# Kernel optimization log

Measured on AMD Instinct MI355X. Metric: run time of the kernel, lower is better.

Reference implementation:

```python
import jax, jax.numpy as jnp
import numpy as np

INPUT_NDIMS = 1024
HIDDEN = 512
LATENT = 50
BATCH = 16384

def setup_inputs() -> dict:
    key = jax.random.key(0)
    ks = jax.random.split(key, 12)
    s = 0.02
    x = jax.random.uniform(ks[0], (BATCH, INPUT_NDIMS), dtype=jnp.float32)
    u = 0.01 + 0.98 * jax.random.uniform(ks[1], (BATCH, LATENT), dtype=jnp.float32)
    W1 = s * jax.random.normal(ks[2], (HIDDEN, INPUT_NDIMS), dtype=jnp.float32)
    b1 = jnp.zeros((HIDDEN,), jnp.float32)
    Wa = s * jax.random.normal(ks[3], (LATENT, HIDDEN), dtype=jnp.float32)
    ba = jnp.zeros((LATENT,), jnp.float32)
    Wb = s * jax.random.normal(ks[4], (LATENT, HIDDEN), dtype=jnp.float32)
    bb = jnp.zeros((LATENT,), jnp.float32)
    W2 = s * jax.random.normal(ks[5], (HIDDEN, LATENT), dtype=jnp.float32)
    b2 = jnp.zeros((HIDDEN,), jnp.float32)
    W3 = s * jax.random.normal(ks[6], (INPUT_NDIMS, HIDDEN), dtype=jnp.float32)
    b3 = jnp.zeros((INPUT_NDIMS,), jnp.float32)
    return dict(x=x, u=u, W1=W1, b1=b1, Wa=Wa, ba=ba, Wb=Wb, bb=bb, W2=W2, b2=b2, W3=W3, b3=b3)

def _stick_segments(v):
    # pi[:, k] = v[:, k] * prod_{j<k} (1 - v[:, j])  -- single O(K) cumprod pass
    cp = jnp.cumprod(1.0 - v, axis=1)                       # inclusive cumprod
    excl = jnp.concatenate([jnp.ones_like(cp[:, :1]), cp[:, :-1]], axis=1)
    return v * excl

def reference(x, u, W1, b1, Wa, ba, Wb, bb, W2, b2, W3, b3):
    # encoder: MLP -> positive Kumaraswamy params alpha (param1), beta (param2)
    h = jax.nn.relu(x @ W1.T + b1)                           # [B, H]
    alpha = jax.nn.softplus(h @ Wa.T + ba) + 1e-4            # [B, K]
    beta = jax.nn.softplus(h @ Wb.T + bb) + 1e-4             # [B, K]
    # Kumaraswamy reparameterized sample: v = (1 - u^(1/beta))^(1/alpha)
    v = jnp.power(1.0 - jnp.power(u, 1.0 / beta), 1.0 / alpha)
    # set_v_K_to_one: force last stick fraction to 1 so segments sum to 1
    v = v.at[:, -1].set(1.0)
    pi = _stick_segments(v)                                  # [B, K], rows sum to 1
    # decoder: MLP with sigmoid output
    h2 = jax.nn.relu(pi @ W2.T + b2)                         # [B, H]
    recon = jax.nn.sigmoid(h2 @ W3.T + b3)                   # [B, D]
    return recon, alpha, beta
```

## Files before the change

### kernel.cpp

```cpp
#include <hip/hip_runtime.h>
#include <hip/hip_bf16.h>

typedef __hip_bfloat16 bf16_t;
typedef __attribute__((ext_vector_type(4))) float f32x4;
typedef __attribute__((ext_vector_type(8))) __bf16 bf16x8;
typedef __attribute__((ext_vector_type(8))) short s16x8;
typedef __attribute__((ext_vector_type(4))) unsigned short u16x4;

#define BATCH 16384
#define NDIM  1024
#define HID   512
#define LAT   50

#define LOG2E 1.44269504088896340736f
#define RLOG2E 0.69314718055994530942f

__device__ __forceinline__ float ex2(float x) { return __builtin_amdgcn_exp2f(x); }
__device__ __forceinline__ float lg2(float x) { return __builtin_amdgcn_logf(x); }
__device__ __forceinline__ float rcp(float x) { return __builtin_amdgcn_rcpf(x); }

__device__ inline unsigned short f2b_u(float f) {
  union { bf16_t b; unsigned short u; } cv; cv.b = __float2bfloat16(f); return cv.u;
}

__device__ __forceinline__ void gload16(const void* src, void* dst_lds) {
  __builtin_amdgcn_global_load_lds(
      reinterpret_cast<const __attribute__((address_space(1))) void*>(
          reinterpret_cast<unsigned long long>(src)),
      reinterpret_cast<__attribute__((address_space(3))) void*>(
          static_cast<unsigned>(reinterpret_cast<unsigned long long>(dst_lds))),
      16, 0, 0);
}

#define WAIT_VMCNT(N)                                          \
  do {                                                         \
    asm volatile("s_waitcnt vmcnt(%0)" ::"i"(N) : "memory");   \
    __builtin_amdgcn_sched_barrier(0);                         \
  } while (0)
#define WAIT_LGKM0                                             \
  do {                                                         \
    asm volatile("s_waitcnt lgkmcnt(0)" ::: "memory");         \
    __builtin_amdgcn_sched_barrier(0);                         \
  } while (0)

__global__ void prep_w_kernel(const float* __restrict__ W1, const float* __restrict__ W3,
                              const float* __restrict__ Wa, const float* __restrict__ Wb,
                              const float* __restrict__ W2, const float* __restrict__ ba,
                              const float* __restrict__ bb,
                              bf16_t* __restrict__ w1, bf16_t* __restrict__ w3,
                              bf16_t* __restrict__ wab, bf16_t* __restrict__ w2p,
                              float* __restrict__ bab)
{
  const int W1U  = (HID * NDIM) / 4;
  const int W3U  = (NDIM * HID) / 4;
  const int WABN = 128 * HID;
  const int W2PN = HID * 64;
  const int TOT  = W1U + W3U + WABN + W2PN + 128;
  for (int i = blockIdx.x * blockDim.x + threadIdx.x; i < TOT;
       i += gridDim.x * blockDim.x) {
    int j = i;
    if (j < W1U) {
      const f32x4 v = ((const f32x4*)W1)[j];
      u16x4 o; o[0]=f2b_u(v[0]); o[1]=f2b_u(v[1]); o[2]=f2b_u(v[2]); o[3]=f2b_u(v[3]);
      ((u16x4*)w1)[j] = o; continue;
    }
    j -= W1U;
    if (j < W3U) {
      const f32x4 v = ((const f32x4*)W3)[j];
      u16x4 o; o[0]=f2b_u(v[0]); o[1]=f2b_u(v[1]); o[2]=f2b_u(v[2]); o[3]=f2b_u(v[3]);
      ((u16x4*)w3)[j] = o; continue;
    }
    j -= W3U;
    if (j < WABN) {
      const int n = j >> 9, k = j & 511;
      float v = (n < 50) ? Wa[n * 512 + k] : ((n < 100) ? Wb[(n - 50) * 512 + k] : 0.f);
      wab[j] = __float2bfloat16(v); continue;
    }
    j -= WABN;
    if (j < W2PN) {
      const int n = j >> 6, k = j & 63;
      w2p[j] = __float2bfloat16(k < 50 ? W2[n * 50 + k] : 0.f); continue;
    }
    j -= W2PN;
    bab[j] = (j < 50) ? ba[j] : ((j < 100) ? bb[j - 50] : 0.f);
  }
}

template<int A_F32, int EPI, int BM>
__global__ __launch_bounds__(512, 1)
void gemm256_kernel(const void* __restrict__ Av, const bf16_t* __restrict__ B,
                    const float* __restrict__ bias, void* __restrict__ out0,
                    int M, int N, int K)
{
  constexpr int BN  = 256;
  constexpr int BUF = (BM + BN) * 128;
  constexpr int RA  = BM / 64;
  constexpr int MI  = BM / 32;
  constexpr int FPQ = MI / 4;
  __shared__ char lds[2 * BUF];

  const int tid  = threadIdx.x;
  const int swzid = ((blockIdx.x & 7) * (gridDim.x >> 3)) + (blockIdx.x >> 3);
  const int nblocks = N / BN;
  const int bn   = swzid % nblocks;
  const int bm   = swzid / nblocks;
  const int wid  = tid >> 6;
  const int lane = tid & 63;
  const int l15  = lane & 15;
  const int l4   = lane >> 4;
  const int wm   = (wid >> 2) * (BM / 2);
  const int wn   = (wid & 3) * 64;
  const int uw   = __builtin_amdgcn_readfirstlane(wid);

  f32x4 acc[MI][4] = {};
  f32x4 areg[4];

  auto stage_A_round = [&](char* buf, int k0, int i) {
    const bf16_t* A = (const bf16_t*)Av;
    const int c  = (i * 8 + uw) * 64 + lane;
    const int r  = c >> 3;
    const int sp = c & 7;
    const int sl = sp ^ (r & 7);
    gload16(A + (size_t)(bm * BM + r) * K + k0 + sl * 8,
            buf + (i * 8 + uw) * 1024);
  };
  auto stage_B_round = [&](char* buf, int k0, int i) {
    char* lB = buf + BM * 128;
    const int c  = (i * 8 + uw) * 64 + lane;
    const int r  = c >> 3;
    const int sp = c & 7;
    const int sl = sp ^ (r & 7);
    gload16(B + (size_t)(bn * BN + r) * K + k0 + sl * 8,
            lB + (i * 8 + uw) * 1024);
  };
  auto load_A_f32 = [&](int k0) {
    const float* A = (const float*)Av;
    #pragma unroll
    for (int j = 0; j < 2; ++j) {
      const int c  = j * 512 + tid;
      const int r  = c >> 3;
      const int sl = c & 7;
      const float* s = A + (size_t)(bm * BM + r) * K + k0 + sl * 8;
      areg[2 * j]     = *(const f32x4*)s;
      areg[2 * j + 1] = *(const f32x4*)(s + 4);
    }
  };
  auto write_A_f32 = [&](char* buf) {
    #pragma unroll
    for (int j = 0; j < 2; ++j) {
      const int c  = j * 512 + tid;
      const int r  = c >> 3;
      const int sl = c & 7;
      const int sp = sl ^ (r & 7);
      union { s16x8 v; unsigned short us[8]; } o;
      const f32x4 v0 = areg[2 * j], v1 = areg[2 * j + 1];
      o.us[0]=f2b_u(v0[0]); o.us[1]=f2b_u(v0[1]); o.us[2]=f2b_u(v0[2]); o.us[3]=f2b_u(v0[3]);
      o.us[4]=f2b_u(v1[0]); o.us[5]=f2b_u(v1[1]); o.us[6]=f2b_u(v1[2]); o.us[7]=f2b_u(v1[3]);
      *(s16x8*)(buf + r * 128 + sp * 16) = o.v;
    }
  };

  const int nt = K >> 6;
  if constexpr (A_F32) {
    load_A_f32(0); write_A_f32(lds);
  } else {
    #pragma unroll
    for (int i = 0; i < RA; ++i) stage_A_round(lds, 0, i);
  }
  #pragma unroll
  for (int i = 0; i < 4; ++i) stage_B_round(lds, 0, i);
  WAIT_VMCNT(0);
  if (A_F32) WAIT_LGKM0;
  __builtin_amdgcn_s_barrier();

  for (int t = 0; t < nt; ++t) {
    char* buf  = lds + (t & 1) * BUF;
    char* nbuf = lds + ((t + 1) & 1) * BUF;
    const char* lA = buf;
    const char* lB = buf + BM * 128;
    const bool pf  = (t + 1 < nt);
    const int k0n  = (t + 1) << 6;

    if (pf) {
      if constexpr (A_F32) {
        load_A_f32(k0n);
      } else {
        #pragma unroll
        for (int i = 0; i < RA; ++i) stage_A_round(nbuf, k0n, i);
      }
      #pragma unroll
      for (int i = 0; i < 4; ++i) stage_B_round(nbuf, k0n, i);
    }

    bf16x8 bfr[4][2];
    #pragma unroll
    for (int ni = 0; ni < 4; ++ni)
      #pragma unroll
      for (int h = 0; h < 2; ++h) {
        const int row = wn + ni * 16 + l15;
        const int sp  = (h * 4 + l4) ^ (row & 7);
        bfr[ni][h] = *(const bf16x8*)(lB + row * 128 + sp * 16);
      }

    #pragma unroll
    for (int q = 0; q < 4; ++q) {
      bf16x8 af[FPQ][2];
      #pragma unroll
      for (int f = 0; f < FPQ; ++f)
        #pragma unroll
        for (int h = 0; h < 2; ++h) {
          const int row = wm + (q * FPQ + f) * 16 + l15;
          const int sp  = (h * 4 + l4) ^ (row & 7);
          af[f][h] = *(const bf16x8*)(lA + row * 128 + sp * 16);
        }
      __builtin_amdgcn_s_setprio(1);
      #pragma unroll
      for (int f = 0; f < FPQ; ++f)
        #pragma unroll
        for (int ni = 0; ni < 4; ++ni)
          #pragma unroll
          for (int h = 0; h < 2; ++h)
            acc[q * FPQ + f][ni] = __builtin_amdgcn_mfma_f32_16x16x32_bf16(
                af[f][h], bfr[ni][h], acc[q * FPQ + f][ni], 0, 0, 0);
      __builtin_amdgcn_s_setprio(0);
    }

    if (A_F32 && pf) write_A_f32(nbuf);
    WAIT_VMCNT(0);
    if (A_F32) WAIT_LGKM0;
    __builtin_amdgcn_s_barrier();
  }

  #pragma unroll
  for (int ni = 0; ni < 4; ++ni) {
    const int n  = bn * BN + wn + ni * 16 + l15;
    const float bv = bias[n];
    #pragma unroll
    for (int mi = 0; mi < MI; ++mi) {
      #pragma unroll
      for (int r = 0; r < 4; ++r) {
        const int m  = bm * BM + wm + mi * 16 + l4 * 4 + r;
        const float t = acc[mi][ni][r] + bv;
        if (EPI == 0) {
          ((bf16_t*)out0)[(size_t)m * N + n] = __float2bfloat16(fmaxf(t, 0.f));
        } else {
          ((float*)out0)[(size_t)m * N + n] = rcp(1.f + ex2(-t * LOG2E));
        }
      }
    }
  }
}

__global__ __launch_bounds__(512, 1)
void abstick_kernel(const bf16_t* __restrict__ A, const bf16_t* __restrict__ wabg,
                    const float* __restrict__ bab, const bf16_t* __restrict__ w2pg,
                    const float* __restrict__ b2, const float* __restrict__ u,
                    float* __restrict__ out_a, float* __restrict__ out_b,
                    bf16_t* __restrict__ h2)
{
  constexpr int BUF = 64 * 128 + 16384;
  constexpr int PIL = 65536;
  constexpr int SMO = 73728;
  __shared__ char lds[100352];

  const int tid  = threadIdx.x;
  const int swzid = ((blockIdx.x & 7) * (gridDim.x >> 3)) + (blockIdx.x >> 3);
  const int bm   = swzid;
  const int wid  = tid >> 6;
  const int lane = tid & 63;
  const int l15  = lane & 15;
  const int l4   = lane >> 4;
  const int wm   = (wid >> 2) * 32;
  const int wn   = (wid & 3) * 32;
  const int uw   = __builtin_amdgcn_readfirstlane(wid);
  const int K    = HID;

  f32x4 acc[2][2] = {};

  auto stage_AB = [&](char* buf, int k0) {
    {
      const int c  = tid;
      const int r  = c >> 3;
      const int sp = c & 7;
      const int sl = sp ^ (r & 7);
      gload16(A + (size_t)(bm * 64 + r) * K + k0 + sl * 8, buf + uw * 1024);
    }
    char* lB = buf + 8192;
    #pragma unroll
    for (int i = 0; i < 2; ++i) {
      const int c  = (i * 8 + uw) * 64 + lane;
      const int r  = c >> 3;
      const int sp = c & 7;
      const int sl = sp ^ (r & 7);
      gload16(wabg + (size_t)r * K + k0 + sl * 8, lB + (i * 8 + uw) * 1024);
    }
  };
  auto compute1 = [&](const char* buf) {
    const char* lA = buf;
    const char* lB = buf + 8192;
    #pragma unroll
    for (int h = 0; h < 2; ++h) {
      bf16x8 af[2], bfr[2];
      #pragma unroll
      for (int mi = 0; mi < 2; ++mi) {
        const int row = wm + mi * 16 + l15;
        const int sp  = (h * 4 + l4) ^ (row & 7);
        af[mi] = *(const bf16x8*)(lA + row * 128 + sp * 16);
      }
      #pragma unroll
      for (int ni = 0; ni < 2; ++ni) {
        const int row = wn + ni * 16 + l15;
        const int sp  = (h * 4 + l4) ^ (row & 7);
        bfr[ni] = *(const bf16x8*)(lB + row * 128 + sp * 16);
      }
      #pragma unroll
      for (int mi = 0; mi < 2; ++mi)
        #pragma unroll
        for (int ni = 0; ni < 2; ++ni)
          acc[mi][ni] = __builtin_amdgcn_mfma_f32_16x16x32_bf16(
              af[mi], bfr[ni], acc[mi][ni], 0, 0, 0);
    }
  };

  stage_AB(lds, 0);
  stage_AB(lds + BUF, 64);
  for (int t = 0; t < 8; ++t) {
    if (t + 1 < 8) WAIT_VMCNT(3);
    else           WAIT_VMCNT(0);
    __builtin_amdgcn_s_barrier();
    compute1(lds + (t & 1) * BUF);
    __builtin_amdgcn_s_barrier();
    __builtin_amdgcn_sched_barrier(0);
    if (t + 2 < 8) stage_AB(lds + (t & 1) * BUF, (t + 2) << 6);
  }

  const int ul = (lane < 49) ? lane : 0;
  float ureg[8];
  #pragma unroll
  for (int rr = 0; rr < 8; ++rr) {
    const size_t m = (size_t)(bm * 64 + wid * 8 + rr);
    ureg[rr] = u[m * 50 + ul];
  }

  #pragma unroll
  for (int i = 0; i < 8; ++i) {
    const int c  = (i * 8 + uw) * 64 + lane;
    const int r  = c >> 3;
    const int sp = c & 7;
    const int sl = sp ^ (r & 7);
    gload16(w2pg + (size_t)r * 64 + sl * 8, lds + (i * 8 + uw) * 1024);
  }

  float* sm = (float*)(lds + SMO);
  #pragma unroll
  for (int ni = 0; ni < 2; ++ni) {
    const int n  = wn + ni * 16 + l15;
    const float bv = bab[n];
    #pragma unroll
    for (int mi = 0; mi < 2; ++mi) {
      #pragma unroll
      for (int r = 0; r < 4; ++r) {
        const int ml = wm + mi * 16 + l4 * 4 + r;
        const int m  = bm * 64 + ml;
        const float t = acc[mi][ni][r] + bv;
        if (n < 100) {
          const float y =
              (t > 20.f ? t : lg2(1.f + ex2(t * LOG2E)) * RLOG2E) + 1e-4f;
          if (n < 50) out_a[(size_t)m * 50 + n] = y;
          else        out_b[(size_t)m * 50 + (n - 50)] = y;
          sm[ml * 104 + n + (n < 50 ? 0 : 2)] = y;
        }
      }
    }
  }
  __syncthreads();

  #pragma unroll 1
  for (int rr = 0; rr < 8; ++rr) {
    const int rl = wid * 8 + rr;
    const size_t m = (size_t)(bm * 64 + rl);
    float v = 1.f, t = 1.f;
    if (lane < 49) {
      const float a  = sm[rl * 104 + lane];
      const float b  = sm[rl * 104 + 52 + lane];
      const float uu = ureg[rr];
      const float tb = ex2(lg2(uu) * rcp(b));
      v = ex2(lg2(1.f - tb) * rcp(a));
      t = 1.f - v;
    }
    float p = t;
    #pragma unroll
    for (int d = 1; d < 64; d <<= 1) {
      const float o = __shfl_up(p, d, 64);
      if (lane >= d) p *= o;
    }
    float e = __shfl_up(p, 1, 64);
    if (lane == 0) e = 1.f;
    const float piv = (lane < 50) ? v * e : 0.f;
    *(unsigned short*)(lds + PIL + rl * 128 +
                       (((lane >> 3) ^ (rl & 7)) << 4) + ((lane & 7) << 1)) =
        f2b_u(piv);
  }
  __syncthreads();

  const int wn3 = (wid & 3) * 128;
  f32x4 acc3[2][8] = {};
  #pragma unroll
  for (int h = 0; h < 2; ++h) {
    bf16x8 af[2], bfr[8];
    #pragma unroll
    for (int mi = 0; mi < 2; ++mi) {
      const int row = wm + mi * 16 + l15;
      const int sp  = (h * 4 + l4) ^ (row & 7);
      af[mi] = *(const bf16x8*)(lds + PIL + row * 128 + sp * 16);
    }
    #pragma unroll
    for (int ni = 0; ni < 8; ++ni) {
      const int row = wn3 + ni * 16 + l15;
      const int sp  = (h * 4 + l4) ^ (row & 7);
      bfr[ni] = *(const bf16x8*)(lds + row * 128 + sp * 16);
    }
    #pragma unroll
    for (int mi = 0; mi < 2; ++mi)
      #pragma unroll
      for (int ni = 0; ni < 8; ++ni)
        acc3[mi][ni] = __builtin_amdgcn_mfma_f32_16x16x32_bf16(
            af[mi], bfr[ni], acc3[mi][ni], 0, 0, 0);
  }
  #pragma unroll
  for (int ni = 0; ni < 8; ++ni) {
    const int n  = wn3 + ni * 16 + l15;
    const float bv = b2[n];
    #pragma unroll
    for (int mi = 0; mi < 2; ++mi) {
      #pragma unroll
      for (int r = 0; r < 4; ++r) {
        const int m  = bm * 64 + wm + mi * 16 + l4 * 4 + r;
        h2[(size_t)m * HID + n] =
            __float2bfloat16(fmaxf(acc3[mi][ni][r] + bv, 0.f));
      }
    }
  }
}

extern "C" void kernel_launch(void* const* d_in, const int* in_sizes, int n_in,
                              void* d_out, int out_size, void* d_ws, size_t ws_size,
                              hipStream_t stream)
{
  const float* x  = (const float*)d_in[0];
  const float* u  = (const float*)d_in[1];
  const float* W1 = (const float*)d_in[2];
  const float* b1 = (const float*)d_in[3];
  const float* Wa = (const float*)d_in[4];
  const float* ba = (const float*)d_in[5];
  const float* Wb = (const float*)d_in[6];
  const float* bb = (const float*)d_in[7];
  const float* W2 = (const float*)d_in[8];
  const float* b2 = (const float*)d_in[9];
  const float* W3 = (const float*)d_in[10];
  const float* b3 = (const float*)d_in[11];

  float* recon  = (float*)d_out;
  float* oalpha = recon + (size_t)BATCH * NDIM;
  float* obeta  = oalpha + (size_t)BATCH * LAT;

  char* ws = (char*)d_ws;
  bf16_t* h2  = (bf16_t*)(ws);
  bf16_t* h   = (bf16_t*)(ws + 16777216);
  bf16_t* w1  = (bf16_t*)(ws + 33554432);
  bf16_t* w3  = (bf16_t*)(ws + 34603008);
  bf16_t* wab = (bf16_t*)(ws + 35651584);
  bf16_t* w2p = (bf16_t*)(ws + 35782656);
  float*  bab = (float*)(ws + 35848192);

  prep_w_kernel<<<512, 256, 0, stream>>>(W1, W3, Wa, Wb, W2, ba, bb,
                                         w1, w3, wab, w2p, bab);
  gemm256_kernel<1, 0, 128><<<256, 512, 0, stream>>>(
      x, w1, b1, (void*)h, BATCH, HID, NDIM);
  abstick_kernel<<<256, 512, 0, stream>>>(
      h, wab, bab, w2p, b2, u, oalpha, obeta, h2);
  gemm256_kernel<0, 1, 256><<<256, 512, 0, stream>>>(
      h2, w3, b3, (void*)recon, BATCH, NDIM, HID);
}
```

Measured before the change: 78.19 us.

## Merge four kernels into one cooperative persistent kernel with grid syncs

Replaces the weight-prep, first GEMM, alpha/beta+stick-breaking, and output GEMM launches with a single cooperative kernel that separates the phases with grid.sync(). The aim is to remove per-launch overhead and inter-kernel gaps. The cost is grid-wide barriers and a larger fixed LDS allocation (128 KB) shared across all phases. The weight prep phase now runs on 256 blocks of 512 threads instead of 512 blocks of 256.

```diff
diff --git a/kernel.cpp b/kernel.cpp
--- a/kernel.cpp
+++ b/kernel.cpp
@@ -1,5 +1,8 @@
 #include <hip/hip_runtime.h>
 #include <hip/hip_bf16.h>
+#include <hip/hip_cooperative_groups.h>
+
+namespace cg = cooperative_groups;
 
 typedef __hip_bfloat16 bf16_t;
 typedef __attribute__((ext_vector_type(4))) float f32x4;
@@ -43,63 +46,18 @@
     __builtin_amdgcn_sched_barrier(0);                         \
   } while (0)
 
-__global__ void prep_w_kernel(const float* __restrict__ W1, const float* __restrict__ W3,
-                              const float* __restrict__ Wa, const float* __restrict__ Wb,
-                              const float* __restrict__ W2, const float* __restrict__ ba,
-                              const float* __restrict__ bb,
-                              bf16_t* __restrict__ w1, bf16_t* __restrict__ w3,
-                              bf16_t* __restrict__ wab, bf16_t* __restrict__ w2p,
-                              float* __restrict__ bab)
-{
-  const int W1U  = (HID * NDIM) / 4;
-  const int W3U  = (NDIM * HID) / 4;
-  const int WABN = 128 * HID;
-  const int W2PN = HID * 64;
-  const int TOT  = W1U + W3U + WABN + W2PN + 128;
-  for (int i = blockIdx.x * blockDim.x + threadIdx.x; i < TOT;
-       i += gridDim.x * blockDim.x) {
-    int j = i;
-    if (j < W1U) {
-      const f32x4 v = ((const f32x4*)W1)[j];
-      u16x4 o; o[0]=f2b_u(v[0]); o[1]=f2b_u(v[1]); o[2]=f2b_u(v[2]); o[3]=f2b_u(v[3]);
-      ((u16x4*)w1)[j] = o; continue;
-    }
-    j -= W1U;
-    if (j < W3U) {
-      const f32x4 v = ((const f32x4*)W3)[j];
-      u16x4 o; o[0]=f2b_u(v[0]); o[1]=f2b_u(v[1]); o[2]=f2b_u(v[2]); o[3]=f2b_u(v[3]);
-      ((u16x4*)w3)[j] = o; continue;
-    }
-    j -= W3U;
-    if (j < WABN) {
-      const int n = j >> 9, k = j & 511;
-      float v = (n < 50) ? Wa[n * 512 + k] : ((n < 100) ? Wb[(n - 50) * 512 + k] : 0.f);
-      wab[j] = __float2bfloat16(v); continue;
-    }
-    j -= WABN;
-    if (j < W2PN) {
-      const int n = j >> 6, k = j & 63;
-      w2p[j] = __float2bfloat16(k < 50 ? W2[n * 50 + k] : 0.f); continue;
-    }
-    j -= W2PN;
-    bab[j] = (j < 50) ? ba[j] : ((j < 100) ? bb[j - 50] : 0.f);
-  }
-}
-
 template<int A_F32, int EPI, int BM>
-__global__ __launch_bounds__(512, 1)
-void gemm256_kernel(const void* __restrict__ Av, const bf16_t* __restrict__ B,
-                    const float* __restrict__ bias, void* __restrict__ out0,
-                    int M, int N, int K)
+__device__ __forceinline__
+void gemm_phase(const void* __restrict__ Av, const bf16_t* __restrict__ B,
+                const float* __restrict__ bias, void* __restrict__ out0,
+                int N, int K, char* lds, int tid)
 {
   constexpr int BN  = 256;
   constexpr int BUF = (BM + BN) * 128;
   constexpr int RA  = BM / 64;
   constexpr int MI  = BM / 32;
   constexpr int FPQ = MI / 4;
-  __shared__ char lds[2 * BUF];
-
-  const int tid  = threadIdx.x;
+
   const int swzid = ((blockIdx.x & 7) * (gridDim.x >> 3)) + (blockIdx.x >> 3);
   const int nblocks = N / BN;
   const int bn   = swzid % nblocks;
@@ -252,195 +210,247 @@
 }
 
 __global__ __launch_bounds__(512, 1)
-void abstick_kernel(const bf16_t* __restrict__ A, const bf16_t* __restrict__ wabg,
-                    const float* __restrict__ bab, const bf16_t* __restrict__ w2pg,
-                    const float* __restrict__ b2, const float* __restrict__ u,
-                    float* __restrict__ out_a, float* __restrict__ out_b,
-                    bf16_t* __restrict__ h2)
+void mega_kernel(const float* __restrict__ x, const float* __restrict__ u,
+                 const float* __restrict__ W1, const float* __restrict__ b1,
+                 const float* __restrict__ Wa, const float* __restrict__ ba,
+                 const float* __restrict__ Wb, const float* __restrict__ bb,
+                 const float* __restrict__ W2, const float* __restrict__ b2,
+                 const float* __restrict__ W3, const float* __restrict__ b3,
+                 float* __restrict__ recon, float* __restrict__ oalpha,
+                 float* __restrict__ obeta, bf16_t* __restrict__ h,
+                 bf16_t* __restrict__ h2, bf16_t* __restrict__ w1,
+                 bf16_t* __restrict__ w3, bf16_t* __restrict__ wab,
+                 bf16_t* __restrict__ w2p, float* __restrict__ bab)
 {
-  constexpr int BUF = 64 * 128 + 16384;
-  constexpr int PIL = 65536;
-  constexpr int SMO = 73728;
-  __shared__ char lds[100352];
-
-  const int tid  = threadIdx.x;
-  const int swzid = ((blockIdx.x & 7) * (gridDim.x >> 3)) + (blockIdx.x >> 3);
-  const int bm   = swzid;
-  const int wid  = tid >> 6;
-  const int lane = tid & 63;
-  const int l15  = lane & 15;
-  const int l4   = lane >> 4;
-  const int wm   = (wid >> 2) * 32;
-  const int wn   = (wid & 3) * 32;
-  const int uw   = __builtin_amdgcn_readfirstlane(wid);
-  const int K    = HID;
-
-  f32x4 acc[2][2] = {};
-
-  auto stage_AB = [&](char* buf, int k0) {
-    {
-      const int c  = tid;
-      const int r  = c >> 3;
-      const int sp = c & 7;
-      const int sl = sp ^ (r & 7);
-      gload16(A + (size_t)(bm * 64 + r) * K + k0 + sl * 8, buf + uw * 1024);
-    }
-    char* lB = buf + 8192;
-    #pragma unroll
-    for (int i = 0; i < 2; ++i) {
+  cg::grid_group grid = cg::this_grid();
+  __shared__ char lds[131072];
+  const int tid = threadIdx.x;
+
+  {
+    const int W1U  = (HID * NDIM) / 4;
+    const int W3U  = (NDIM * HID) / 4;
+    const int WABN = 128 * HID;
+    const int W2PN = HID * 64;
+    const int TOT  = W1U + W3U + WABN + W2PN + 128;
+    for (int i = blockIdx.x * blockDim.x + tid; i < TOT;
+         i += gridDim.x * blockDim.x) {
+      int j = i;
+      if (j < W1U) {
+        const f32x4 v = ((const f32x4*)W1)[j];
+        u16x4 o; o[0]=f2b_u(v[0]); o[1]=f2b_u(v[1]); o[2]=f2b_u(v[2]); o[3]=f2b_u(v[3]);
+        ((u16x4*)w1)[j] = o; continue;
+      }
+      j -= W1U;
+      if (j < W3U) {
+        const f32x4 v = ((const f32x4*)W3)[j];
+        u16x4 o; o[0]=f2b_u(v[0]); o[1]=f2b_u(v[1]); o[2]=f2b_u(v[2]); o[3]=f2b_u(v[3]);
+        ((u16x4*)w3)[j] = o; continue;
+      }
+      j -= W3U;
+      if (j < WABN) {
+        const int n = j >> 9, k = j & 511;
+        float v = (n < 50) ? Wa[n * 512 + k] : ((n < 100) ? Wb[(n - 50) * 512 + k] : 0.f);
+        wab[j] = __float2bfloat16(v); continue;
+      }
+      j -= WABN;
+      if (j < W2PN) {
+        const int n = j >> 6, k = j & 63;
+        w2p[j] = __float2bfloat16(k < 50 ? W2[n * 50 + k] : 0.f); continue;
+      }
+      j -= W2PN;
+      bab[j] = (j < 50) ? ba[j] : ((j < 100) ? bb[j - 50] : 0.f);
+    }
+  }
+  grid.sync();
+
+  gemm_phase<1, 0, 128>(x, w1, b1, (void*)h, HID, NDIM, lds, tid);
+  grid.sync();
+
+  {
+    constexpr int BUF = 64 * 128 + 16384;
+    constexpr int PIL = 65536;
+    constexpr int SMO = 73728;
+    const bf16_t* A = h;
+    const int swzid = ((blockIdx.x & 7) * (gridDim.x >> 3)) + (blockIdx.x >> 3);
+    const int bm   = swzid;
+    const int wid  = tid >> 6;
+    const int lane = tid & 63;
+    const int l15  = lane & 15;
+    const int l4   = lane >> 4;
+    const int wm   = (wid >> 2) * 32;
+    const int wn   = (wid & 3) * 32;
+    const int uw   = __builtin_amdgcn_readfirstlane(wid);
+    const int K    = HID;
+
+    f32x4 acc[2][2] = {};
+
+    auto stage_AB = [&](char* buf, int k0) {
+      {
+        const int c  = tid;
+        const int r  = c >> 3;
+        const int sp = c & 7;
+        const int sl = sp ^ (r & 7);
+        gload16(A + (size_t)(bm * 64 + r) * K + k0 + sl * 8, buf + uw * 1024);
+      }
+      char* lB = buf + 8192;
+      #pragma unroll
+      for (int i = 0; i < 2; ++i) {
+        const int c  = (i * 8 + uw) * 64 + lane;
+        const int r  = c >> 3;
+        const int sp = c & 7;
+        const int sl = sp ^ (r & 7);
+        gload16(wab + (size_t)r * K + k0 + sl * 8, lB + (i * 8 + uw) * 1024);
+      }
+    };
+    auto compute1 = [&](const char* buf) {
+      const char* lA = buf;
+      const char* lB = buf + 8192;
+      #pragma unroll
+      for (int hh = 0; hh < 2; ++hh) {
+        bf16x8 af[2], bfr[2];
+        #pragma unroll
+        for (int mi = 0; mi < 2; ++mi) {
+          const int row = wm + mi * 16 + l15;
+          const int sp  = (hh * 4 + l4) ^ (row & 7);
+          af[mi] = *(const bf16x8*)(lA + row * 128 + sp * 16);
+        }
+        #pragma unroll
+        for (int ni = 0; ni < 2; ++ni) {
+          const int row = wn + ni * 16 + l15;
+          const int sp  = (hh * 4 + l4) ^ (row & 7);
+          bfr[ni] = *(const bf16x8*)(lB + row * 128 + sp * 16);
+        }
+        #pragma unroll
+        for (int mi = 0; mi < 2; ++mi)
+          #pragma unroll
+          for (int ni = 0; ni < 2; ++ni)
+            acc[mi][ni] = __builtin_amdgcn_mfma_f32_16x16x32_bf16(
+                af[mi], bfr[ni], acc[mi][ni], 0, 0, 0);
+      }
+    };
+
+    stage_AB(lds, 0);
+    stage_AB(lds + BUF, 64);
+    for (int t = 0; t < 8; ++t) {
+      if (t + 1 < 8) WAIT_VMCNT(3);
+      else           WAIT_VMCNT(0);
+      __builtin_amdgcn_s_barrier();
+      compute1(lds + (t & 1) * BUF);
+      __builtin_amdgcn_s_barrier();
+      __builtin_amdgcn_sched_barrier(0);
+      if (t + 2 < 8) stage_AB(lds + (t & 1) * BUF, (t + 2) << 6);
+    }
+
+    const int ul = (lane < 49) ? lane : 0;
+    float ureg[8];
+    #pragma unroll
+    for (int rr = 0; rr < 8; ++rr) {
+      const size_t m = (size_t)(bm * 64 + wid * 8 + rr);
+      ureg[rr] = u[m * 50 + ul];
+    }
+
+    #pragma unroll
+    for (int i = 0; i < 8; ++i) {
       const int c  = (i * 8 + uw) * 64 + lane;
       const int r  = c >> 3;
       const int sp = c & 7;
       const int sl = sp ^ (r & 7);
-      gload16(wabg + (size_t)r * K + k0 + sl * 8, lB + (i * 8 + uw) * 1024);
-    }
-  };
-  auto compute1 = [&](const char* buf) {
-    const char* lA = buf;
-    const char* lB = buf + 8192;
-    #pragma unroll
-    for (int h = 0; h < 2; ++h) {
-      bf16x8 af[2], bfr[2];
+      gload16(w2p + (size_t)r * 64 + sl * 8, lds + (i * 8 + uw) * 1024);
+    }
+
+    float* sm = (float*)(lds + SMO);
+    #pragma unroll
+    for (int ni = 0; ni < 2; ++ni) {
+      const int n  = wn + ni * 16 + l15;
+      const float bv = bab[n];
+      #pragma unroll
+      for (int mi = 0; mi < 2; ++mi) {
+        #pragma unroll
+        for (int r = 0; r < 4; ++r) {
+          const int ml = wm + mi * 16 + l4 * 4 + r;
+          const int m  = bm * 64 + ml;
+          const float t = acc[mi][ni][r] + bv;
+          if (n < 100) {
+            const float y =
+                (t > 20.f ? t : lg2(1.f + ex2(t * LOG2E)) * RLOG2E) + 1e-4f;
+            if (n < 50) oalpha[(size_t)m * 50 + n] = y;
+            else        obeta[(size_t)m * 50 + (n - 50)] = y;
+            sm[ml * 104 + n + (n < 50 ? 0 : 2)] = y;
+          }
+        }
+      }
+    }
+    __syncthreads();
+
+    #pragma unroll 1
+    for (int rr = 0; rr < 8; ++rr) {
+      const int rl = wid * 8 + rr;
+      float v = 1.f, t = 1.f;
+      if (lane < 49) {
+        const float a  = sm[rl * 104 + lane];
+        const float b  = sm[rl * 104 + 52 + lane];
+        const float uu = ureg[rr];
+        const float tb = ex2(lg2(uu) * rcp(b));
+        v = ex2(lg2(1.f - tb) * rcp(a));
+        t = 1.f - v;
+      }
+      float p = t;
+      #pragma unroll
+      for (int d = 1; d < 64; d <<= 1) {
+        const float o = __shfl_up(p, d, 64);
+        if (lane >= d) p *= o;
+      }
+      float e = __shfl_up(p, 1, 64);
+      if (lane == 0) e = 1.f;
+      const float piv = (lane < 50) ? v * e : 0.f;
+      *(unsigned short*)(lds + PIL + rl * 128 +
+                         (((lane >> 3) ^ (rl & 7)) << 4) + ((lane & 7) << 1)) =
+          f2b_u(piv);
+    }
+    __syncthreads();
+
+    const int wn3 = (wid & 3) * 128;
+    f32x4 acc3[2][8] = {};
+    #pragma unroll
+    for (int hh = 0; hh < 2; ++hh) {
+      bf16x8 af[2], bfr[8];
       #pragma unroll
       for (int mi = 0; mi < 2; ++mi) {
         const int row = wm + mi * 16 + l15;
-        const int sp  = (h * 4 + l4) ^ (row & 7);
-        af[mi] = *(const bf16x8*)(lA + row * 128 + sp * 16);
-      }
-      #pragma unroll
-      for (int ni = 0; ni < 2; ++ni) {
-        const int row = wn + ni * 16 + l15;
-        const int sp  = (h * 4 + l4) ^ (row & 7);
-        bfr[ni] = *(const bf16x8*)(lB + row * 128 + sp * 16);
+        const int sp  = (hh * 4 + l4) ^ (row & 7);
+        af[mi] = *(const bf16x8*)(lds + PIL + row * 128 + sp * 16);
+      }
+      #pragma unroll
+      for (int ni = 0; ni < 8; ++ni) {
+        const int row = wn3 + ni * 16 + l15;
+        const int sp  = (hh * 4 + l4) ^ (row & 7);
+        bfr[ni] = *(const bf16x8*)(lds + row * 128 + sp * 16);
       }
       #pragma unroll
       for (int mi = 0; mi < 2; ++mi)
         #pragma unroll
-        for (int ni = 0; ni < 2; ++ni)
-          acc[mi][ni] = __builtin_amdgcn_mfma_f32_16x16x32_bf16(
-              af[mi], bfr[ni], acc[mi][ni], 0, 0, 0);
-    }
-  };
-
-  stage_AB(lds, 0);
-  stage_AB(lds + BUF, 64);
-  for (int t = 0; t < 8; ++t) {
-    if (t + 1 < 8) WAIT_VMCNT(3);
-    else           WAIT_VMCNT(0);
-    __builtin_amdgcn_s_barrier();
-    compute1(lds + (t & 1) * BUF);
-    __builtin_amdgcn_s_barrier();
-    __builtin_amdgcn_sched_barrier(0);
-    if (t + 2 < 8) stage_AB(lds + (t & 1) * BUF, (t + 2) << 6);
+        for (int ni = 0; ni < 8; ++ni)
+          acc3[mi][ni] = __builtin_amdgcn_mfma_f32_16x16x32_bf16(
+              af[mi], bfr[ni], acc3[mi][ni], 0, 0, 0);
+    }
+    #pragma unroll
+    for (int ni = 0; ni < 8; ++ni) {
+      const int n  = wn3 + ni * 16 + l15;
+      const float bv = b2[n];
+      #pragma unroll
+      for (int mi = 0; mi < 2; ++mi) {
+        #pragma unroll
+        for (int r = 0; r < 4; ++r) {
+          const int m  = bm * 64 + wm + mi * 16 + l4 * 4 + r;
+          h2[(size_t)m * HID + n] =
+              __float2bfloat16(fmaxf(acc3[mi][ni][r] + bv, 0.f));
+        }
+      }
+    }
   }
-
-  const int ul = (lane < 49) ? lane : 0;
-  float ureg[8];
-  #pragma unroll
-  for (int rr = 0; rr < 8; ++rr) {
-    const size_t m = (size_t)(bm * 64 + wid * 8 + rr);
-    ureg[rr] = u[m * 50 + ul];
-  }
-
-  #pragma unroll
-  for (int i = 0; i < 8; ++i) {
-    const int c  = (i * 8 + uw) * 64 + lane;
-    const int r  = c >> 3;
-    const int sp = c & 7;
-    const int sl = sp ^ (r & 7);
-    gload16(w2pg + (size_t)r * 64 + sl * 8, lds + (i * 8 + uw) * 1024);
-  }
-
-  float* sm = (float*)(lds + SMO);
-  #pragma unroll
-  for (int ni = 0; ni < 2; ++ni) {
-    const int n  = wn + ni * 16 + l15;
-    const float bv = bab[n];
-    #pragma unroll
-    for (int mi = 0; mi < 2; ++mi) {
-      #pragma unroll
-      for (int r = 0; r < 4; ++r) {
-        const int ml = wm + mi * 16 + l4 * 4 + r;
-        const int m  = bm * 64 + ml;
-        const float t = acc[mi][ni][r] + bv;
-        if (n < 100) {
-          const float y =
-              (t > 20.f ? t : lg2(1.f + ex2(t * LOG2E)) * RLOG2E) + 1e-4f;
-          if (n < 50) out_a[(size_t)m * 50 + n] = y;
-          else        out_b[(size_t)m * 50 + (n - 50)] = y;
-          sm[ml * 104 + n + (n < 50 ? 0 : 2)] = y;
-        }
-      }
-    }
-  }
-  __syncthreads();
-
-  #pragma unroll 1
-  for (int rr = 0; rr < 8; ++rr) {
-    const int rl = wid * 8 + rr;
-    const size_t m = (size_t)(bm * 64 + rl);
-    float v = 1.f, t = 1.f;
-    if (lane < 49) {
-      const float a  = sm[rl * 104 + lane];
-      const float b  = sm[rl * 104 + 52 + lane];
-      const float uu = ureg[rr];
-      const float tb = ex2(lg2(uu) * rcp(b));
-      v = ex2(lg2(1.f - tb) * rcp(a));
-      t = 1.f - v;
-    }
-    float p = t;
-    #pragma unroll
-    for (int d = 1; d < 64; d <<= 1) {
-      const float o = __shfl_up(p, d, 64);
-      if (lane >= d) p *= o;
-    }
-    float e = __shfl_up(p, 1, 64);
-    if (lane == 0) e = 1.f;
-    const float piv = (lane < 50) ? v * e : 0.f;
-    *(unsigned short*)(lds + PIL + rl * 128 +
-                       (((lane >> 3) ^ (rl & 7)) << 4) + ((lane & 7) << 1)) =
-        f2b_u(piv);
-  }
-  __syncthreads();
-
-  const int wn3 = (wid & 3) * 128;
-  f32x4 acc3[2][8] = {};
-  #pragma unroll
-  for (int h = 0; h < 2; ++h) {
-    bf16x8 af[2], bfr[8];
-    #pragma unroll
-    for (int mi = 0; mi < 2; ++mi) {
-      const int row = wm + mi * 16 + l15;
-      const int sp  = (h * 4 + l4) ^ (row & 7);
-      af[mi] = *(const bf16x8*)(lds + PIL + row * 128 + sp * 16);
-    }
-    #pragma unroll
-    for (int ni = 0; ni < 8; ++ni) {
-      const int row = wn3 + ni * 16 + l15;
-      const int sp  = (h * 4 + l4) ^ (row & 7);
-      bfr[ni] = *(const bf16x8*)(lds + row * 128 + sp * 16);
-    }
-    #pragma unroll
-    for (int mi = 0; mi < 2; ++mi)
-      #pragma unroll
-      for (int ni = 0; ni < 8; ++ni)
-        acc3[mi][ni] = __builtin_amdgcn_mfma_f32_16x16x32_bf16(
-            af[mi], bfr[ni], acc3[mi][ni], 0, 0, 0);
-  }
-  #pragma unroll
-  for (int ni = 0; ni < 8; ++ni) {
-    const int n  = wn3 + ni * 16 + l15;
-    const float bv = b2[n];
-    #pragma unroll
-    for (int mi = 0; mi < 2; ++mi) {
-      #pragma unroll
-      for (int r = 0; r < 4; ++r) {
-        const int m  = bm * 64 + wm + mi * 16 + l4 * 4 + r;
-        h2[(size_t)m * HID + n] =
-            __float2bfloat16(fmaxf(acc3[mi][ni][r] + bv, 0.f));
-      }
-    }
-  }
+  grid.sync();
+
+  gemm_phase<0, 1, 256>(h2, w3, b3, (void*)recon, NDIM, HID, lds, tid);
 }
 
 extern "C" void kernel_launch(void* const* d_in, const int* in_sizes, int n_in,
@@ -473,12 +483,11 @@
   bf16_t* w2p = (bf16_t*)(ws + 35782656);
   float*  bab = (float*)(ws + 35848192);
 
-  prep_w_kernel<<<512, 256, 0, stream>>>(W1, W3, Wa, Wb, W2, ba, bb,
-                                         w1, w3, wab, w2p, bab);
-  gemm256_kernel<1, 0, 128><<<256, 512, 0, stream>>>(
-      x, w1, b1, (void*)h, BATCH, HID, NDIM);
-  abstick_kernel<<<256, 512, 0, stream>>>(
-      h, wab, bab, w2p, b2, u, oalpha, obeta, h2);
-  gemm256_kernel<0, 1, 256><<<256, 512, 0, stream>>>(
-      h2, w3, b3, (void*)recon, BATCH, NDIM, HID);
+  void* kargs[] = {
+      (void*)&x,  (void*)&u,  (void*)&W1, (void*)&b1, (void*)&Wa, (void*)&ba,
+      (void*)&Wb, (void*)&bb, (void*)&W2, (void*)&b2, (void*)&W3, (void*)&b3,
+      (void*)&recon, (void*)&oalpha, (void*)&obeta, (void*)&h, (void*)&h2,
+      (void*)&w1, (void*)&w3, (void*)&wab, (void*)&w2p, (void*)&bab};
+  hipLaunchCooperativeKernel((const void*)mega_kernel, dim3(256), dim3(512),
+                             kargs, 0, stream);
 }
```

New measurement: 179.6 us, median of 4. 130% more time.
